# Optimization experiments

Hardware: AMD Instinct MI355X
Metric: run time of the kernel (lower is better)

## Reference

```python
import jax, jax.numpy as jnp
import numpy as np

TABLE_NUM = 16
TABLE_SIZE_LOG2 = 12
T = 1 << TABLE_SIZE_LOG2          # 4096 entries per table
FEAT = 2                          # features per entry (mini_linear in = table_num*2)
Z_DIM = 512
RES_MIN = 16
RES_MAX = 256
IMG = 256
MLP_HIDDEN = 64
OUT_DIM = 3
BATCH = 8
PRIME_Y = np.uint32(2654435761)   # instant-NGP spatial hash prime


def setup_inputs() -> dict:
    key = jax.random.key(0)
    ks = jax.random.split(key, 9)
    d_tab = TABLE_NUM * T * FEAT
    return {
        "z": jax.random.normal(ks[0], (BATCH, Z_DIM), jnp.float32),
        "w_table": jax.random.normal(ks[1], (Z_DIM, d_tab), jnp.float32) * 1e-2,
        "b_table": jnp.zeros((d_tab,), jnp.float32),
        "w1": jax.random.normal(ks[2], (TABLE_NUM * FEAT, MLP_HIDDEN), jnp.float32) * (1.0 / np.sqrt(TABLE_NUM * FEAT)),
        "b1": jnp.zeros((MLP_HIDDEN,), jnp.float32),
        "w2": jax.random.normal(ks[3], (MLP_HIDDEN, MLP_HIDDEN), jnp.float32) * (1.0 / np.sqrt(MLP_HIDDEN)),
        "b2": jnp.zeros((MLP_HIDDEN,), jnp.float32),
        "w3": jax.random.normal(ks[4], (MLP_HIDDEN, OUT_DIM), jnp.float32) * (1.0 / np.sqrt(MLP_HIDDEN)),
        "b3": jnp.zeros((OUT_DIM,), jnp.float32),
    }


def _sample_coords(b):
    c = (jnp.arange(IMG, dtype=jnp.float32) + 0.5) / IMG
    xx, yy = jnp.meshgrid(c, c, indexing="ij")  # torch.meshgrid default
    coords = jnp.stack([xx, yy], axis=-1).reshape(1, -1, 2)
    return jnp.broadcast_to(coords, (b, IMG * IMG, 2))


def _hash_retrieve(tables, coords):
    """tables: B x L x T x F; coords: B x N x 2 in [0,1). Returns B x N x (L*F)."""
    B, L, _, _ = tables.shape
    growth = np.exp((np.log(RES_MAX) - np.log(RES_MIN)) / (L - 1))
    offs = jnp.array([[0, 0], [1, 0], [0, 1], [1, 1]], dtype=jnp.uint32)  # 4 corners
    bidx = jnp.arange(B)[:, None, None]
    feats = []
    for l in range(L):
        res = jnp.float32(RES_MIN * (growth ** l))
        pos = coords * res                      # B,N,2
        pos0 = jnp.floor(pos)
        frac = pos - pos0                       # B,N,2
        corner = pos0.astype(jnp.uint32)[:, :, None, :] + offs[None, None]  # B,N,4,2
        idx = (corner[..., 0] ^ (corner[..., 1] * PRIME_Y)) & jnp.uint32(T - 1)
        f = tables[:, l][bidx, idx.astype(jnp.int32)]        # B,N,4,F gather
        fx, fy = frac[..., 0], frac[..., 1]
        w = jnp.stack([(1 - fx) * (1 - fy), fx * (1 - fy),
                       (1 - fx) * fy,       fx * fy], axis=-1)  # B,N,4
        feats.append(jnp.einsum("bncf,bnc->bnf", f, w))
    return jnp.concatenate(feats, axis=-1)


def reference(z, w_table, b_table, w1, b1, w2, b2, w3, b3):
    B = z.shape[0]
    tables = (z @ w_table + b_table).reshape(B, TABLE_NUM, T, FEAT)
    coords = _sample_coords(B).astype(tables.dtype)
    feat = _hash_retrieve(tables, coords)                    # B,N,L*F
    h = jax.nn.relu(feat @ w1 + b1)
    h = jax.nn.relu(h @ w2 + b2)
    o = jnp.tanh(h @ w3 + b3)                                # B,N,3
    return o.reshape(B, IMG, IMG, OUT_DIM).transpose(0, 3, 1, 2)
```

## Files before the change

### kernel.cpp

```cpp
#include <hip/hip_runtime.h>
#include <cmath>

#define TABLE_NUM 16
#define T_SIZE    4096
#define Z_DIM     512
#define IMG       256
#define D_TAB     (TABLE_NUM * T_SIZE * 2)
#define BATCH     8
#define HID       64
#define N_PIX     (IMG * IMG)
#define PRIME_Y   2654435761u

typedef _Float16 v8h  __attribute__((ext_vector_type(8)));
typedef _Float16 v2h  __attribute__((ext_vector_type(2)));
typedef float    v4f  __attribute__((ext_vector_type(4)));

struct ResArr { float r[TABLE_NUM]; };

__global__ void prep_weights(const float* __restrict__ w1, const float* __restrict__ w2,
                             const float* __restrict__ w3,
                             _Float16* __restrict__ w1T, _Float16* __restrict__ w2T,
                             _Float16* __restrict__ w3T)
{
    const int t = threadIdx.x;
    for (int i = t; i < HID * 32; i += 256) {
        int n = i >> 5, k = i & 31;
        w1T[i] = (_Float16)w1[k * HID + n];
    }
    for (int i = t; i < HID * HID; i += 256) {
        int n = i >> 6, k = i & 63;
        w2T[i] = (_Float16)w2[k * HID + n];
    }
    for (int i = t; i < 16 * HID; i += 256) {
        int n = i >> 6, k = i & 63;
        w3T[i] = (_Float16)(n < 3 ? w3[k * 3 + n] : 0.f);
    }
}

__global__ __launch_bounds__(256) void gen_tables(
    const float* __restrict__ z, const float* __restrict__ w,
    const float* __restrict__ bt, float* __restrict__ tabs)
{
    const int n = blockIdx.x * 256 + threadIdx.x;
    float acc[BATCH];
#pragma unroll
    for (int b = 0; b < BATCH; ++b) acc[b] = 0.f;

#pragma unroll 16
    for (int k = 0; k < Z_DIM; ++k) {
        float wv = w[(size_t)k * D_TAB + n];
#pragma unroll
        for (int b = 0; b < BATCH; ++b)
            acc[b] = fmaf(z[b * Z_DIM + k], wv, acc[b]);
    }

    float bv = bt[n];
#pragma unroll
    for (int b = 0; b < BATCH; ++b)
        tabs[(size_t)b * D_TAB + n] = acc[b] + bv;
}

__global__ __launch_bounds__(256) void hash_mlp(
    const float* __restrict__ tabs,
    const _Float16* __restrict__ w1T, const _Float16* __restrict__ w2T,
    const _Float16* __restrict__ w3T,
    const float* __restrict__ b1, const float* __restrict__ b2,
    const float* __restrict__ b3,
    float* __restrict__ out, ResArr res)
{
    __shared__ _Float16 mbuf[4][64][72];
    const int tid  = threadIdx.x;
    const int wid  = tid >> 6;
    const int lane = tid & 63;
    const int b    = blockIdx.x & 7;
    const int tile = blockIdx.x >> 3;
    const int ti   = tile >> 4;
    const int tj   = tile & 15;
    const int i0   = ti * 16 + wid * 4;
    const int j0   = tj * 16;

    const int di = lane >> 4, dj = lane & 15;
    const float cx = ((float)(i0 + di) + 0.5f) * (1.0f / IMG);
    const float cy = ((float)(j0 + dj) + 0.5f) * (1.0f / IMG);
    const float* tb = tabs + (size_t)b * D_TAB;
    const float2* tb2 = reinterpret_cast<const float2*>(tb);

#pragma unroll 4
    for (int l = 0; l < TABLE_NUM; ++l) {
        float r  = res.r[l];
        float px = cx * r, py = cy * r;
        float fx0 = floorf(px), fy0 = floorf(py);
        float fx = px - fx0, fy = py - fy0;
        unsigned x0 = (unsigned)(int)fx0, y0 = (unsigned)(int)fy0;
        unsigned hy0 = y0 * PRIME_Y, hy1 = (y0 + 1u) * PRIME_Y;
        unsigned i00 = (x0 ^ hy0) & (T_SIZE - 1);
        unsigned i10 = ((x0 + 1u) ^ hy0) & (T_SIZE - 1);
        unsigned i01 = (x0 ^ hy1) & (T_SIZE - 1);
        unsigned i11 = ((x0 + 1u) ^ hy1) & (T_SIZE - 1);
        const float2* tl = tb2 + l * T_SIZE;
        float2 f00 = tl[i00], f10 = tl[i10], f01 = tl[i01], f11 = tl[i11];
        float w00 = (1.f - fx) * (1.f - fy);
        float w10 = fx * (1.f - fy);
        float w01 = (1.f - fx) * fy;
        float w11 = fx * fy;
        float e0 = f00.x * w00 + f10.x * w10 + f01.x * w01 + f11.x * w11;
        float e1 = f00.y * w00 + f10.y * w10 + f01.y * w01 + f11.y * w11;
        v2h p; p.x = (_Float16)e0; p.y = (_Float16)e1;
        *reinterpret_cast<v2h*>(&mbuf[wid][lane][2 * l]) = p;
    }

    const int arow = lane & 15;
    const int kgrp = lane >> 4;

    float bias1v[4], bias2v[4];
#pragma unroll
    for (int nt = 0; nt < 4; ++nt) {
        bias1v[nt] = b1[nt * 16 + arow];
        bias2v[nt] = b2[nt * 16 + arow];
    }
    const float bias3 = (arow < 3) ? b3[arow] : 0.f;

    v8h bf1[4], bf2a[4], bf2b[4];
#pragma unroll
    for (int nt = 0; nt < 4; ++nt) {
        bf1[nt]  = *reinterpret_cast<const v8h*>(&w1T[(nt * 16 + arow) * 32 + kgrp * 8]);
        bf2a[nt] = *reinterpret_cast<const v8h*>(&w2T[(nt * 16 + arow) * 64 + kgrp * 8]);
        bf2b[nt] = *reinterpret_cast<const v8h*>(&w2T[(nt * 16 + arow) * 64 + 32 + kgrp * 8]);
    }
    v8h bf3a = *reinterpret_cast<const v8h*>(&w3T[arow * 64 + kgrp * 8]);
    v8h bf3b = *reinterpret_cast<const v8h*>(&w3T[arow * 64 + 32 + kgrp * 8]);

    v8h a1[4];
#pragma unroll
    for (int mt = 0; mt < 4; ++mt)
        a1[mt] = *reinterpret_cast<const v8h*>(&mbuf[wid][mt * 16 + arow][kgrp * 8]);

    v4f c1[4][4];
#pragma unroll
    for (int nt = 0; nt < 4; ++nt)
#pragma unroll
        for (int mt = 0; mt < 4; ++mt) {
            v4f c = {0.f, 0.f, 0.f, 0.f};
            c = __builtin_amdgcn_mfma_f32_16x16x32_f16(a1[mt], bf1[nt], c, 0, 0, 0);
#pragma unroll
            for (int e = 0; e < 4; ++e)
                c1[mt][nt][e] = fmaxf(c[e] + bias1v[nt], 0.f);
        }

#pragma unroll
    for (int mt = 0; mt < 4; ++mt)
#pragma unroll
        for (int nt = 0; nt < 4; ++nt)
#pragma unroll
            for (int e = 0; e < 4; ++e)
                mbuf[wid][mt * 16 + kgrp * 4 + e][nt * 16 + arow] = (_Float16)c1[mt][nt][e];

    v8h a2[4][2];
#pragma unroll
    for (int mt = 0; mt < 4; ++mt) {
        a2[mt][0] = *reinterpret_cast<const v8h*>(&mbuf[wid][mt * 16 + arow][kgrp * 8]);
        a2[mt][1] = *reinterpret_cast<const v8h*>(&mbuf[wid][mt * 16 + arow][32 + kgrp * 8]);
    }
    v4f c2[4][4];
#pragma unroll
    for (int nt = 0; nt < 4; ++nt)
#pragma unroll
        for (int mt = 0; mt < 4; ++mt) {
            v4f c = {0.f, 0.f, 0.f, 0.f};
            c = __builtin_amdgcn_mfma_f32_16x16x32_f16(a2[mt][0], bf2a[nt], c, 0, 0, 0);
            c = __builtin_amdgcn_mfma_f32_16x16x32_f16(a2[mt][1], bf2b[nt], c, 0, 0, 0);
#pragma unroll
            for (int e = 0; e < 4; ++e)
                c2[mt][nt][e] = fmaxf(c[e] + bias2v[nt], 0.f);
        }

#pragma unroll
    for (int mt = 0; mt < 4; ++mt)
#pragma unroll
        for (int nt = 0; nt < 4; ++nt)
#pragma unroll
            for (int e = 0; e < 4; ++e)
                mbuf[wid][mt * 16 + kgrp * 4 + e][nt * 16 + arow] = (_Float16)c2[mt][nt][e];

#pragma unroll
    for (int mt = 0; mt < 4; ++mt) {
        v8h a0  = *reinterpret_cast<const v8h*>(&mbuf[wid][mt * 16 + arow][kgrp * 8]);
        v8h a1v = *reinterpret_cast<const v8h*>(&mbuf[wid][mt * 16 + arow][32 + kgrp * 8]);
        v4f c = {0.f, 0.f, 0.f, 0.f};
        c = __builtin_amdgcn_mfma_f32_16x16x32_f16(a0,  bf3a, c, 0, 0, 0);
        c = __builtin_amdgcn_mfma_f32_16x16x32_f16(a1v, bf3b, c, 0, 0, 0);
        if (arow < 3) {
            float4 st;
            st.x = tanhf(c[0] + bias3);
            st.y = tanhf(c[1] + bias3);
            st.z = tanhf(c[2] + bias3);
            st.w = tanhf(c[3] + bias3);
            size_t idx = ((size_t)b * 3 + arow) * N_PIX
                       + (size_t)(i0 + mt) * IMG + j0 + kgrp * 4;
            *reinterpret_cast<float4*>(&out[idx]) = st;
        }
    }
}

extern "C" void kernel_launch(void* const* d_in, const int* in_sizes, int n_in,
                              void* d_out, int out_size, void* d_ws, size_t ws_size,
                              hipStream_t stream)
{
    const float* z  = (const float*)d_in[0];
    const float* wt = (const float*)d_in[1];
    const float* bt = (const float*)d_in[2];
    const float* w1 = (const float*)d_in[3];
    const float* b1 = (const float*)d_in[4];
    const float* w2 = (const float*)d_in[5];
    const float* b2 = (const float*)d_in[6];
    const float* w3 = (const float*)d_in[7];
    const float* b3 = (const float*)d_in[8];
    float* out  = (float*)d_out;

    char* ws = (char*)d_ws;
    float*     tabs = (float*)ws;
    _Float16*  w1T  = (_Float16*)(ws + (4 << 20));
    _Float16*  w2T  = (_Float16*)(ws + (4 << 20) + 4096);
    _Float16*  w3T  = (_Float16*)(ws + (4 << 20) + 12288);

    ResArr ra;
    const double growth = std::exp((std::log(256.0) - std::log(16.0)) / 15.0);
    for (int l = 0; l < TABLE_NUM; ++l)
        ra.r[l] = (float)(16.0 * std::pow(growth, (double)l));

    prep_weights<<<1, 256, 0, stream>>>(w1, w2, w3, w1T, w2T, w3T);
    gen_tables<<<D_TAB / 256, 256, 0, stream>>>(z, wt, bt, tabs);
    hash_mlp<<<BATCH * (N_PIX / 256), 256, 0, stream>>>(
        tabs, w1T, w2T, w3T, b1, b2, b3, out, ra);
}
```

Before: 113.3 us.

## Stage per-tile hash corners in LDS and vectorize table generation

The hash encoding now has each 16x16 pixel block gather the distinct grid corners it needs for each level into a double-buffered shared-memory tile. Pixels then interpolate from LDS instead of issuing four scattered global loads each, so corners shared by neighbouring pixels are fetched once. Table generation now has each thread compute four output columns with float4 loads and stores, using 128-thread blocks. The cost is extra syncthreads per level and a fixed 19x19 staging footprint that relies on the maximum resolution covering at most 17 cells per tile.

Measured after the change: 121.0 us. 6.8% more time.

```diff
diff --git a/kernel.cpp b/kernel.cpp
--- a/kernel.cpp
+++ b/kernel.cpp
@@ -10,6 +10,8 @@
 #define HID       64
 #define N_PIX     (IMG * IMG)
 #define PRIME_Y   2654435761u
+#define CPITCH    19
+#define CBUF      (CPITCH * CPITCH)
 
 typedef _Float16 v8h  __attribute__((ext_vector_type(8)));
 typedef _Float16 v2h  __attribute__((ext_vector_type(2)));
@@ -37,27 +39,40 @@
     }
 }
 
-__global__ __launch_bounds__(256) void gen_tables(
+__global__ __launch_bounds__(128) void gen_tables(
     const float* __restrict__ z, const float* __restrict__ w,
     const float* __restrict__ bt, float* __restrict__ tabs)
 {
-    const int n = blockIdx.x * 256 + threadIdx.x;
-    float acc[BATCH];
-#pragma unroll
-    for (int b = 0; b < BATCH; ++b) acc[b] = 0.f;
+    const int c4 = blockIdx.x * 128 + threadIdx.x;
+    const float4* wp = reinterpret_cast<const float4*>(w) + c4;
+
+    float4 acc[BATCH];
+#pragma unroll
+    for (int b = 0; b < BATCH; ++b) acc[b] = make_float4(0.f, 0.f, 0.f, 0.f);
 
 #pragma unroll 16
     for (int k = 0; k < Z_DIM; ++k) {
-        float wv = w[(size_t)k * D_TAB + n];
-#pragma unroll
-        for (int b = 0; b < BATCH; ++b)
-            acc[b] = fmaf(z[b * Z_DIM + k], wv, acc[b]);
-    }
-
-    float bv = bt[n];
-#pragma unroll
-    for (int b = 0; b < BATCH; ++b)
-        tabs[(size_t)b * D_TAB + n] = acc[b] + bv;
+        float4 wv = wp[(size_t)k * (D_TAB / 4)];
+#pragma unroll
+        for (int b = 0; b < BATCH; ++b) {
+            float zv = z[b * Z_DIM + k];
+            acc[b].x = fmaf(zv, wv.x, acc[b].x);
+            acc[b].y = fmaf(zv, wv.y, acc[b].y);
+            acc[b].z = fmaf(zv, wv.z, acc[b].z);
+            acc[b].w = fmaf(zv, wv.w, acc[b].w);
+        }
+    }
+
+    float4 bv = reinterpret_cast<const float4*>(bt)[c4];
+#pragma unroll
+    for (int b = 0; b < BATCH; ++b) {
+        float4 o;
+        o.x = acc[b].x + bv.x;
+        o.y = acc[b].y + bv.y;
+        o.z = acc[b].z + bv.z;
+        o.w = acc[b].w + bv.w;
+        reinterpret_cast<float4*>(tabs)[(size_t)b * (D_TAB / 4) + c4] = o;
+    }
 }
 
 __global__ __launch_bounds__(256) void hash_mlp(
@@ -69,45 +84,79 @@
     float* __restrict__ out, ResArr res)
 {
     __shared__ _Float16 mbuf[4][64][72];
+    __shared__ float2   cstage[2][CBUF];
+
     const int tid  = threadIdx.x;
     const int wid  = tid >> 6;
     const int lane = tid & 63;
     const int b    = blockIdx.x & 7;
     const int tile = blockIdx.x >> 3;
-    const int ti   = tile >> 4;
-    const int tj   = tile & 15;
-    const int i0   = ti * 16 + wid * 4;
-    const int j0   = tj * 16;
+    const int i0b  = (tile >> 4) * 16;
+    const int j0b  = (tile & 15) * 16;
+    const int i0   = i0b + wid * 4;
 
     const int di = lane >> 4, dj = lane & 15;
-    const float cx = ((float)(i0 + di) + 0.5f) * (1.0f / IMG);
-    const float cy = ((float)(j0 + dj) + 0.5f) * (1.0f / IMG);
-    const float* tb = tabs + (size_t)b * D_TAB;
-    const float2* tb2 = reinterpret_cast<const float2*>(tb);
-
-#pragma unroll 4
+    const float cxp = ((float)(i0 + di) + 0.5f) * (1.0f / IMG);
+    const float cyp = ((float)(j0b + dj) + 0.5f) * (1.0f / IMG);
+    const float2* tb2 = reinterpret_cast<const float2*>(tabs + (size_t)b * D_TAB);
+
+    const float cx_lo = ((float)i0b + 0.5f)  * (1.0f / IMG);
+    const float cx_hi = ((float)i0b + 15.5f) * (1.0f / IMG);
+    const float cy_lo = ((float)j0b + 0.5f)  * (1.0f / IMG);
+    const float cy_hi = ((float)j0b + 15.5f) * (1.0f / IMG);
+
+    const int tx = tid & 15, ty = tid >> 4;
+
+#define STAGE(L, CB)                                                          \
+    {                                                                         \
+        const float r = res.r[L];                                             \
+        const int xs = (int)floorf(cx_lo * r);                                \
+        const int xe = (int)floorf(cx_hi * r) + 1;                            \
+        const int ys = (int)floorf(cy_lo * r);                                \
+        const int ye = (int)floorf(cy_hi * r) + 1;                            \
+        const int W = xe - xs + 1, H = ye - ys + 1;                           \
+        const float2* tl = tb2 + (L) * T_SIZE;                                \
+        for (int yy = ty; yy < H; yy += 16)                                   \
+            for (int xx = tx; xx < W; xx += 16) {                             \
+                unsigned idx = ((unsigned)(xs + xx) ^                         \
+                                ((unsigned)(ys + yy) * PRIME_Y)) & (T_SIZE-1);\
+                (CB)[yy * CPITCH + xx] = tl[idx];                             \
+            }                                                                 \
+    }
+
+#define CONSUME(L, CB)                                                        \
+    {                                                                         \
+        const float r = res.r[L];                                             \
+        const int xs = (int)floorf(cx_lo * r);                                \
+        const int ys = (int)floorf(cy_lo * r);                                \
+        float px = cxp * r, py = cyp * r;                                     \
+        float fx0 = floorf(px), fy0 = floorf(py);                             \
+        float fx = px - fx0, fy = py - fy0;                                   \
+        int xi = (int)fx0 - xs, yi = (int)fy0 - ys;                           \
+        float2 f00 = (CB)[yi * CPITCH + xi];                                  \
+        float2 f10 = (CB)[yi * CPITCH + xi + 1];                              \
+        float2 f01 = (CB)[(yi + 1) * CPITCH + xi];                            \
+        float2 f11 = (CB)[(yi + 1) * CPITCH + xi + 1];                        \
+        float w00 = (1.f - fx) * (1.f - fy);                                  \
+        float w10 = fx * (1.f - fy);                                          \
+        float w01 = (1.f - fx) * fy;                                          \
+        float w11 = fx * fy;                                                  \
+        float e0 = f00.x * w00 + f10.x * w10 + f01.x * w01 + f11.x * w11;     \
+        float e1 = f00.y * w00 + f10.y * w10 + f01.y * w01 + f11.y * w11;     \
+        v2h p; p.x = (_Float16)e0; p.y = (_Float16)e1;                        \
+        *reinterpret_cast<v2h*>(&mbuf[wid][lane][2 * (L)]) = p;               \
+    }
+
+    STAGE(0, cstage[0]);
+    __syncthreads();
+#pragma unroll
     for (int l = 0; l < TABLE_NUM; ++l) {
-        float r  = res.r[l];
-        float px = cx * r, py = cy * r;
-        float fx0 = floorf(px), fy0 = floorf(py);
-        float fx = px - fx0, fy = py - fy0;
-        unsigned x0 = (unsigned)(int)fx0, y0 = (unsigned)(int)fy0;
-        unsigned hy0 = y0 * PRIME_Y, hy1 = (y0 + 1u) * PRIME_Y;
-        unsigned i00 = (x0 ^ hy0) & (T_SIZE - 1);
-        unsigned i10 = ((x0 + 1u) ^ hy0) & (T_SIZE - 1);
-        unsigned i01 = (x0 ^ hy1) & (T_SIZE - 1);
-        unsigned i11 = ((x0 + 1u) ^ hy1) & (T_SIZE - 1);
-        const float2* tl = tb2 + l * T_SIZE;
-        float2 f00 = tl[i00], f10 = tl[i10], f01 = tl[i01], f11 = tl[i11];
-        float w00 = (1.f - fx) * (1.f - fy);
-        float w10 = fx * (1.f - fy);
-        float w01 = (1.f - fx) * fy;
-        float w11 = fx * fy;
-        float e0 = f00.x * w00 + f10.x * w10 + f01.x * w01 + f11.x * w11;
-        float e1 = f00.y * w00 + f10.y * w10 + f01.y * w01 + f11.y * w11;
-        v2h p; p.x = (_Float16)e0; p.y = (_Float16)e1;
-        *reinterpret_cast<v2h*>(&mbuf[wid][lane][2 * l]) = p;
-    }
+        if (l + 1 < TABLE_NUM) STAGE(l + 1, cstage[(l + 1) & 1]);
+        CONSUME(l, cstage[l & 1]);
+        __syncthreads();
+    }
+#undef STAGE
+#undef CONSUME
 
     const int arow = lane & 15;
     const int kgrp = lane >> 4;
@@ -196,7 +245,7 @@
             st.z = tanhf(c[2] + bias3);
             st.w = tanhf(c[3] + bias3);
             size_t idx = ((size_t)b * 3 + arow) * N_PIX
-                       + (size_t)(i0 + mt) * IMG + j0 + kgrp * 4;
+                       + (size_t)(i0 + mt) * IMG + j0b + kgrp * 4;
             *reinterpret_cast<float4*>(&out[idx]) = st;
         }
     }
@@ -229,7 +278,7 @@
         ra.r[l] = (float)(16.0 * std::pow(growth, (double)l));
 
     prep_weights<<<1, 256, 0, stream>>>(w1, w2, w3, w1T, w2T, w3T);
-    gen_tables<<<D_TAB / 256, 256, 0, stream>>>(z, wt, bt, tabs);
+    gen_tables<<<D_TAB / 4 / 128, 128, 0, stream>>>(z, wt, bt, tabs);
     hash_mlp<<<BATCH * (N_PIX / 256), 256, 0, stream>>>(
         tabs, w1T, w2T, w3T, b1, b2, b3, out, ra);
 }
```

## Split table-generation GEMM over K chunks with float4 loads and separate reduce

Applied to the files above, without the earlier changes.

Replaces the single-pass table generation with a split-K scheme: four K chunks each compute float4-wide partial sums into a workspace, and a second kernel sums the partials and adds the bias. z is transposed in the prep kernel so each k step reads its batch values contiguously. The aim is better memory-level parallelism and vectorized reads of the 64 MB weight matrix, which the previous kernel read with too few blocks in flight. The cost is an extra kernel launch and about 16 MB of partial-sum traffic written and read back.

Result: faster. 99.37 us (-12.3%).

```diff
diff --git a/kernel.cpp b/kernel.cpp
--- a/kernel.cpp
+++ b/kernel.cpp
@@ -10,6 +10,9 @@
 #define HID       64
 #define N_PIX     (IMG * IMG)
 #define PRIME_Y   2654435761u
+#define KCHUNK    4
+#define KLEN      (Z_DIM / KCHUNK)
+#define NG4       (D_TAB / 4)
 
 typedef _Float16 v8h  __attribute__((ext_vector_type(8)));
 typedef _Float16 v2h  __attribute__((ext_vector_type(2)));
@@ -18,9 +21,9 @@
 struct ResArr { float r[TABLE_NUM]; };
 
 __global__ void prep_weights(const float* __restrict__ w1, const float* __restrict__ w2,
-                             const float* __restrict__ w3,
+                             const float* __restrict__ w3, const float* __restrict__ z,
                              _Float16* __restrict__ w1T, _Float16* __restrict__ w2T,
-                             _Float16* __restrict__ w3T)
+                             _Float16* __restrict__ w3T, float* __restrict__ zT)
 {
     const int t = threadIdx.x;
     for (int i = t; i < HID * 32; i += 256) {
@@ -35,29 +38,63 @@
         int n = i >> 6, k = i & 63;
         w3T[i] = (_Float16)(n < 3 ? w3[k * 3 + n] : 0.f);
     }
-}
-
-__global__ __launch_bounds__(256) void gen_tables(
-    const float* __restrict__ z, const float* __restrict__ w,
-    const float* __restrict__ bt, float* __restrict__ tabs)
-{
-    const int n = blockIdx.x * 256 + threadIdx.x;
-    float acc[BATCH];
-#pragma unroll
-    for (int b = 0; b < BATCH; ++b) acc[b] = 0.f;
-
-#pragma unroll 16
-    for (int k = 0; k < Z_DIM; ++k) {
-        float wv = w[(size_t)k * D_TAB + n];
-#pragma unroll
-        for (int b = 0; b < BATCH; ++b)
-            acc[b] = fmaf(z[b * Z_DIM + k], wv, acc[b]);
-    }
-
-    float bv = bt[n];
+    for (int i = t; i < Z_DIM * BATCH; i += 256) {
+        int k = i >> 3, b = i & 7;
+        zT[i] = z[b * Z_DIM + k];
+    }
+}
+
+__global__ __launch_bounds__(256) void gen_partial(
+    const float* __restrict__ zT, const float* __restrict__ w,
+    float* __restrict__ part)
+{
+    const int c  = blockIdx.x >> 7;
+    const int g  = (blockIdx.x & 127) * 256 + threadIdx.x;
+    const int k0 = c * KLEN;
+    const float4* wp = reinterpret_cast<const float4*>(w) + g;
+
+    float4 acc[BATCH];
+#pragma unroll
+    for (int b = 0; b < BATCH; ++b) acc[b] = make_float4(0.f, 0.f, 0.f, 0.f);
+
+#pragma unroll 8
+    for (int kk = 0; kk < KLEN; ++kk) {
+        const int k = k0 + kk;
+        float4 wv = wp[(size_t)k * NG4];
+        const float* zr = zT + k * BATCH;
+#pragma unroll
+        for (int b = 0; b < BATCH; ++b) {
+            float zv = zr[b];
+            acc[b].x = fmaf(zv, wv.x, acc[b].x);
+            acc[b].y = fmaf(zv, wv.y, acc[b].y);
+            acc[b].z = fmaf(zv, wv.z, acc[b].z);
+            acc[b].w = fmaf(zv, wv.w, acc[b].w);
+        }
+    }
+
+    float4* pp = reinterpret_cast<float4*>(part);
 #pragma unroll
     for (int b = 0; b < BATCH; ++b)
-        tabs[(size_t)b * D_TAB + n] = acc[b] + bv;
+        pp[((size_t)(c * BATCH + b) << 15) + g] = acc[b];
+}
+
+__global__ __launch_bounds__(256) void gen_reduce(
+    const float* __restrict__ part, const float* __restrict__ bt,
+    float* __restrict__ tabs)
+{
+    const int i = blockIdx.x * 256 + threadIdx.x;
+    const int b = i >> 15, g = i & (NG4 - 1);
+    const float4* pp = reinterpret_cast<const float4*>(part);
+
+    float4 s = pp[((size_t)(0 * BATCH + b) << 15) + g];
+#pragma unroll
+    for (int c = 1; c < KCHUNK; ++c) {
+        float4 p = pp[((size_t)(c * BATCH + b) << 15) + g];
+        s.x += p.x; s.y += p.y; s.z += p.z; s.w += p.w;
+    }
+    float4 bv = reinterpret_cast<const float4*>(bt)[g];
+    s.x += bv.x; s.y += bv.y; s.z += bv.z; s.w += bv.w;
+    reinterpret_cast<float4*>(tabs)[((size_t)b << 15) + g] = s;
 }
 
 __global__ __launch_bounds__(256) void hash_mlp(
@@ -219,17 +256,20 @@
 
     char* ws = (char*)d_ws;
     float*     tabs = (float*)ws;
-    _Float16*  w1T  = (_Float16*)(ws + (4 << 20));
-    _Float16*  w2T  = (_Float16*)(ws + (4 << 20) + 4096);
-    _Float16*  w3T  = (_Float16*)(ws + (4 << 20) + 12288);
+    float*     part = (float*)(ws + (4 << 20));
+    _Float16*  w1T  = (_Float16*)(ws + (20 << 20));
+    _Float16*  w2T  = (_Float16*)(ws + (20 << 20) + 4096);
+    _Float16*  w3T  = (_Float16*)(ws + (20 << 20) + 12288);
+    float*     zT   = (float*)(ws + (20 << 20) + 16384);
 
     ResArr ra;
     const double growth = std::exp((std::log(256.0) - std::log(16.0)) / 15.0);
     for (int l = 0; l < TABLE_NUM; ++l)
         ra.r[l] = (float)(16.0 * std::pow(growth, (double)l));
 
-    prep_weights<<<1, 256, 0, stream>>>(w1, w2, w3, w1T, w2T, w3T);
-    gen_tables<<<D_TAB / 256, 256, 0, stream>>>(z, wt, bt, tabs);
+    prep_weights<<<1, 256, 0, stream>>>(w1, w2, w3, z, w1T, w2T, w3T, zT);
+    gen_partial<<<KCHUNK * (NG4 / 256), 256, 0, stream>>>(zT, wt, part);
+    gen_reduce<<<BATCH * NG4 / 256, 256, 0, stream>>>(part, bt, tabs);
     hash_mlp<<<BATCH * (N_PIX / 256), 256, 0, stream>>>(
         tabs, w1T, w2T, w3T, b1, b2, b3, out, ra);
 }
```
